# Optimization experiments

Measured on AMD Instinct MI355X. Metric: run time of the kernel, lower is better.

The kernel has to match this reference:

```python
import jax, jax.numpy as jnp
import numpy as np

H = 400          # hidden_layers
D_CUR = 3 + 2 + 50   # X_CUR + X_WIN + X_ET
D_AC = 3 + 49        # X_AC + X_T
D_AP = 6 + 49        # X_AP + X_T


def _cell(x, h1, c1, h2, c2, Wx, U, b):
    """2-child child-sum LSTM cell (inferred CustomLSTMCell).
    x: [T, in]; h*/c*: [T, H]; Wx: [in, 4H]; U: [H, 4H]; b: [4H].
    Gate order: i, f, o, u. f uses a per-child recurrent term.
    """
    g = x @ Wx + b                            # [T, 4H]
    gi, gf, go, gu = jnp.split(g, 4, axis=-1)
    Ui, Uf, Uo, Uu = jnp.split(U, 4, axis=-1)
    hs = h1 + h2
    i = jax.nn.sigmoid(gi + hs @ Ui)
    f1 = jax.nn.sigmoid(gf + h1 @ Uf)
    f2 = jax.nn.sigmoid(gf + h2 @ Uf)
    o = jax.nn.sigmoid(go + hs @ Uo)
    u = jnp.tanh(gu + hs @ Uu)
    c = i * u + f1 * c1 + f2 * c2
    return o * jnp.tanh(c), c


def setup_inputs() -> dict:
    key = jax.random.key(0)
    T, IN = 8192, 55
    ks = iter(jax.random.split(key, 40))

    def p(*shape):
        return jax.random.normal(next(ks), shape, dtype=jnp.float32) * 0.05

    inp = {
        "x_temp": jax.random.normal(next(ks), (T, IN), dtype=jnp.float32),
        "x_air": jax.random.normal(next(ks), (T, IN), dtype=jnp.float32),
    }
    for name, d_in in [("t1", IN), ("t2", H), ("t3", H), ("a1", IN), ("a2", H), ("a3", H)]:
        inp[f"Wx_{name}"] = p(d_in, 4 * H)
        inp[f"U_{name}"] = p(H, 4 * H)
        inp[f"b_{name}"] = p(4 * H)
    inp["W_cur"] = p(2 * H, D_CUR); inp["b_cur"] = p(D_CUR)
    inp["W_ac"] = p(H, D_AC);       inp["b_ac"] = p(D_AC)
    inp["W_ap"] = p(H, D_AP);       inp["b_ap"] = p(D_AP)
    return inp


def reference(x_temp, x_air,
              Wx_t1, U_t1, b_t1, Wx_t2, U_t2, b_t2, Wx_t3, U_t3, b_t3,
              Wx_a1, U_a1, b_a1, Wx_a2, U_a2, b_a2, Wx_a3, U_a3, b_a3,
              W_cur, b_cur, W_ac, b_ac, W_ap, b_ap):
    T = x_temp.shape[0]
    z = jnp.zeros((T, H), dtype=x_temp.dtype)
    # States are re-zeroed every timestep in the original loop, so all
    # timesteps are independent and we batch them along axis 0.
    ht, ct = _cell(x_temp, z, z, z, z, Wx_t1, U_t1, b_t1)
    ha, ca = _cell(x_air,  z, z, z, z, Wx_a1, U_a1, b_a1)
    ht2, ct2 = _cell(ht, ht, ct, ha, ca, Wx_t2, U_t2, b_t2)
    ha2, ca2 = _cell(ha, ht, ct, ha, ca, Wx_a2, U_a2, b_a2)
    ht3, _ = _cell(ht2, ht2, ct2, ha2, ca2, Wx_t3, U_t3, b_t3)
    ha3, _ = _cell(ha2, ht2, ct2, ha2, ca2, Wx_a3, U_a3, b_a3)
    out_cur_win_t = jnp.concatenate([ht3, ha3], axis=-1) @ W_cur + b_cur  # [T, 55]
    out_ac_tet = ht3 @ W_ac + b_ac                                        # [T, 52]
    out_ap_aet = ha3 @ W_ap + b_ap                                        # [T, 55]
    return out_cur_win_t, out_ac_tet, out_ap_aet
```

## Files before the change

### kernel.cpp

```cpp
#include <hip/hip_runtime.h>
#include <hip/hip_bf16.h>

typedef unsigned short u16;
typedef unsigned int u32;
typedef unsigned long long u64;
typedef __attribute__((ext_vector_type(4))) float f32x4;
typedef __attribute__((ext_vector_type(8))) short s16x8;

__device__ inline u16 f2bf(float f) {
  union { float f; u32 u; } v; v.f = f;
  u32 r = (v.u + 0x7FFFu + ((v.u >> 16) & 1u)) >> 16;
  return (u16)r;
}
__device__ inline float bf2f(u16 h) { return __uint_as_float((u32)h << 16); }
__device__ inline float sigf(float x) { return 1.0f / (1.0f + __expf(-x)); }
__device__ inline float tanhf_(float x) {
  float ax = fabsf(x);
  float e = __expf(-2.0f * ax);
  float r = (1.0f - e) / (1.0f + e);
  return copysignf(r, x);
}
__device__ inline f32x4 ld4bf(const u16* p) {
  u64 v = *(const u64*)p;
  f32x4 r;
  r.x = __uint_as_float((u32)(v & 0xFFFFu) << 16);
  r.y = __uint_as_float((u32)((v >> 16) & 0xFFFFu) << 16);
  r.z = __uint_as_float((u32)((v >> 32) & 0xFFFFu) << 16);
  r.w = __uint_as_float((u32)((v >> 48) & 0xFFFFu) << 16);
  return r;
}
__device__ inline void gload16(const u16* g, u16* l) {
  __builtin_amdgcn_global_load_lds(
      (const __attribute__((address_space(1))) void*)(g),
      (__attribute__((address_space(3))) void*)(l), 16, 0, 0);
}

#define GLD 4096

__global__ void zero_pads(u16* __restrict__ A1, u16* __restrict__ A2,
                          u16* __restrict__ A3) {
  int idx = blockIdx.x * 256 + threadIdx.x;
  if (idx >= 196608) return;
  int b = idx / 65536, r = idx % 65536;
  int t = r / 8, q = r % 8;
  u16* A = (b == 0) ? A1 : (b == 1) ? A2 : A3;
  *(u64*)(A + (size_t)t * 832 + 800 + q * 4) = 0ULL;
}

__global__ void pad_cast(const float* __restrict__ src, u16* __restrict__ dst,
                         int srcCols, int dstCols, int rows) {
  int idx = blockIdx.x * 256 + threadIdx.x;
  if (idx >= rows * dstCols) return;
  int r = idx / dstCols, c = idx % dstCols;
  float v = (c < srcCols) ? src[r * srcCols + c] : 0.f;
  dst[idx] = f2bf(v);
}

__global__ void transpose_cast(const float* __restrict__ src, u16* __restrict__ dst,
                               int srcK, int srcN) {
  int idx = blockIdx.x * 256 + threadIdx.x;
  if (idx >= 64 * 1664) return;
  int k = idx / 1664, n = idx % 1664;
  float v = (k < srcK && n < srcN) ? src[k * srcN + n] : 0.f;
  dst[n * 64 + k] = f2bf(v);
}

__global__ __launch_bounds__(256) void build_cell_B(
    const float* __restrict__ WxT, const float* __restrict__ UT,
    const float* __restrict__ WxA, const float* __restrict__ UA,
    u16* __restrict__ dst) {
  __shared__ float tile[64][65];
  const int np0 = blockIdx.x * 64;
  const int r0 = blockIdx.y * 64;
  const int tx = threadIdx.x & 63, ty = threadIdx.x >> 6;

  const int np = np0 + tx;
  const int cell = np >> 11;
  const int n = np & 2047;
  const float* Wx = cell ? WxA : WxT;
  const float* U  = cell ? UA  : UT;
  int g = 0, j = 0, gc = 0;
  if (n < 2000) {
    g = n / 400; j = n % 400;
    gc = (g == 0) ? j : (g <= 2) ? 400 + j : (g == 3) ? 800 + j : 1200 + j;
  }
#pragma unroll
  for (int it = 0; it < 16; ++it) {
    int r = r0 + it * 4 + ty;
    float v = 0.f;
    if (n < 2000 && r < 800) {
      bool htside = (r < 400);
      int rr = htside ? r : r - 400;
      float wx = Wx[rr * 1600 + gc];
      float uu = U [rr * 1600 + gc];
      if (cell == 0) {
        if (htside) v = (g == 2) ? wx : wx + uu;
        else        v = (g == 1) ? 0.f : uu;
      } else {
        if (htside) v = (g == 2) ? 0.f : uu;
        else        v = (g == 1) ? wx : wx + uu;
      }
    }
    tile[tx][it * 4 + ty] = v;
  }
  __syncthreads();
#pragma unroll
  for (int it = 0; it < 16; ++it) {
    int npw = np0 + it * 4 + ty;
    dst[(size_t)npw * 832 + r0 + tx] = f2bf(tile[it * 4 + ty][tx]);
  }
}

__global__ void build_proj_B(const float* __restrict__ Wcur, const float* __restrict__ Wac,
                             const float* __restrict__ Wap, u16* __restrict__ dst) {
  int idx = blockIdx.x * 256 + threadIdx.x;
  if (idx >= 256 * 832) return;
  int n = idx / 832, r = idx % 832;
  float v = 0.f;
  if (r < 800) {
    if (n < 55) v = Wcur[r * 55 + n];
    else if (n < 107) { if (r < 400) v = Wac[r * 52 + (n - 55)]; }
    else if (n < 162) { if (r >= 400) v = Wap[(r - 400) * 55 + (n - 107)]; }
  }
  dst[idx] = f2bf(v);
}

__global__ __launch_bounds__(256) void gemm_lds(
    const u16* __restrict__ A, const u16* __restrict__ Bt,
    u16* __restrict__ C, int K, int ldc) {
  __shared__ u16 As[128 * 64];
  __shared__ u16 Bs[128 * 64];
  const int tid = threadIdx.x;
  const int lane = tid & 63;
  const int wid = tid >> 6;

  const int nwg = gridDim.x * gridDim.y;
  const int bid = blockIdx.y * gridDim.x + blockIdx.x;
  const int swz = (bid & 7) * (nwg >> 3) + (bid >> 3);
  const int m0 = (swz / gridDim.x) * 128;
  const int n0 = (swz % gridDim.x) * 128;

  const int wm = (wid >> 1) << 6;
  const int wn = (wid & 1) << 6;

  f32x4 acc[4][4];
#pragma unroll
  for (int i = 0; i < 4; ++i)
#pragma unroll
    for (int j = 0; j < 4; ++j) acc[i][j] = (f32x4){0.f, 0.f, 0.f, 0.f};

  const int nkt = K >> 6;
  const int l8 = lane >> 3, lb = lane & 7;
  const int scol = (lb ^ l8) << 3;
  const u16* gA = A + (size_t)(m0 + wid * 8 + l8) * K + scol;
  const u16* gB = Bt + (size_t)(n0 + wid * 8 + l8) * K + scol;
  u16* lA = As + wid * 8 * 64;
  u16* lB = Bs + wid * 8 * 64;

  const int kq = (lane >> 4) << 3;
  const int rrow = lane & 15;

  for (int kt = 0; kt < nkt; ++kt) {
    __syncthreads();
    const u16* pa = gA + kt * 64;
    const u16* pb = gB + kt * 64;
#pragma unroll
    for (int c = 0; c < 4; ++c) {
      gload16(pa + (size_t)(c * 32) * K, lA + c * 2048);
      gload16(pb + (size_t)(c * 32) * K, lB + c * 2048);
    }
    __syncthreads();
#pragma unroll
    for (int half = 0; half < 2; ++half) {
      const int kk = half * 32 + kq;
      s16x8 af[4], bfr[4];
#pragma unroll
      for (int f = 0; f < 4; ++f) {
        int ar = wm + f * 16 + rrow;
        af[f] = *(const s16x8*)((const char*)As + ar * 128 + ((kk * 2) ^ ((ar & 7) << 4)));
        int br = wn + f * 16 + rrow;
        bfr[f] = *(const s16x8*)((const char*)Bs + br * 128 + ((kk * 2) ^ ((br & 7) << 4)));
      }
#pragma unroll
      for (int i = 0; i < 4; ++i)
#pragma unroll
        for (int j = 0; j < 4; ++j)
          acc[i][j] = __builtin_amdgcn_mfma_f32_16x16x32_bf16(af[i], bfr[j], acc[i][j], 0, 0, 0);
    }
  }

  const int crow0 = m0 + wm + ((lane >> 4) << 2);
  const int ccol0 = n0 + wn + rrow;
#pragma unroll
  for (int i = 0; i < 4; ++i)
#pragma unroll
    for (int j = 0; j < 4; ++j)
#pragma unroll
      for (int r = 0; r < 4; ++r)
        C[(size_t)(crow0 + i * 16 + r) * ldc + (ccol0 + j * 16)] = f2bf(acc[i][j][r]);
}

#define PK 832
#define PNKT 13
#define ABY 32768
#define BBY 16384
#define BUFB 49152

__global__ __launch_bounds__(512, 2) void gemm_pipe(
    const u16* __restrict__ A, const u16* __restrict__ Bt,
    u16* __restrict__ C, int ldc) {
  __shared__ char sm[3 * BUFB];
  const int tid = threadIdx.x;
  const int lane = tid & 63;
  const int wid = tid >> 6;

  const int nwg = gridDim.x * gridDim.y;
  const int bid = blockIdx.y * gridDim.x + blockIdx.x;
  const int swz = (bid & 7) * (nwg >> 3) + (bid >> 3);
  const int m0 = (swz / gridDim.x) * 256;
  const int n0 = (swz % gridDim.x) * 128;

  const int wr = wid >> 1;
  const int wc = wid & 1;

  f32x4 acc[4][4];
#pragma unroll
  for (int i = 0; i < 4; ++i)
#pragma unroll
    for (int j = 0; j < 4; ++j) acc[i][j] = (f32x4){0.f, 0.f, 0.f, 0.f};

  const int q = lane >> 3, lb = lane & 7;
  const int scol = (lb ^ q) << 3;
  const u16* gA = A + (size_t)(m0 + wid * 8 + q) * PK + scol;
  const u16* gB = Bt + (size_t)(n0 + wid * 8 + q) * PK + scol;
  const int wrow = wid * 8;

  const int kq = (lane >> 4) << 3;
  const int rrow = lane & 15;

#define STAGE(kt, buf)                                                        \
  {                                                                           \
    char* bb = sm + (buf) * BUFB;                                             \
    const u16* pa = gA + (kt) * 64;                                           \
    const u16* pb = gB + (kt) * 64;                                           \
    gload16(pa,                  (u16*)(bb + (0 * 64 + wrow) * 128));         \
    gload16(pa + 64 * PK,        (u16*)(bb + (1 * 64 + wrow) * 128));         \
    gload16(pa + 128 * PK,       (u16*)(bb + (2 * 64 + wrow) * 128));         \
    gload16(pa + 192 * PK,       (u16*)(bb + (3 * 64 + wrow) * 128));         \
    gload16(pb,                  (u16*)(bb + ABY + (0 * 64 + wrow) * 128));   \
    gload16(pb + 64 * PK,        (u16*)(bb + ABY + (1 * 64 + wrow) * 128));   \
  }

  STAGE(0, 0);
  STAGE(1, 1);

  int cbuf = 0;
  int sbuf = 2;
  for (int k = 0; k < PNKT; ++k) {
    __builtin_amdgcn_sched_barrier(0);
    __builtin_amdgcn_s_barrier();
    if (k < PNKT - 2) {
      STAGE(k + 2, sbuf);
      asm volatile("s_waitcnt vmcnt(12)" ::: "memory");
    } else if (k == PNKT - 2) {
      asm volatile("s_waitcnt vmcnt(6)" ::: "memory");
    } else {
      asm volatile("s_waitcnt vmcnt(0)" ::: "memory");
    }
    __builtin_amdgcn_s_barrier();
    __builtin_amdgcn_sched_barrier(0);

    const char* bb = sm + cbuf * BUFB;
    s16x8 af[4][2], bfr[4][2];
#pragma unroll
    for (int i = 0; i < 4; ++i) {
      int ar = wr * 64 + i * 16 + rrow;
      const char* base = bb + ar * 128;
#pragma unroll
      for (int h = 0; h < 2; ++h) {
        int kk2 = (h * 32 + kq) * 2;
        af[i][h] = *(const s16x8*)(base + (kk2 ^ ((ar & 7) << 4)));
      }
    }
#pragma unroll
    for (int jf = 0; jf < 4; ++jf) {
      int br = wc * 64 + jf * 16 + rrow;
      const char* base = bb + ABY + br * 128;
#pragma unroll
      for (int h = 0; h < 2; ++h) {
        int kk2 = (h * 32 + kq) * 2;
        bfr[jf][h] = *(const s16x8*)(base + (kk2 ^ ((br & 7) << 4)));
      }
    }
#pragma unroll
    for (int i = 0; i < 4; ++i)
#pragma unroll
      for (int jf = 0; jf < 4; ++jf)
#pragma unroll
        for (int h = 0; h < 2; ++h)
          acc[i][jf] = __builtin_amdgcn_mfma_f32_16x16x32_bf16(
              af[i][h], bfr[jf][h], acc[i][jf], 0, 0, 0);

    cbuf = (cbuf == 2) ? 0 : cbuf + 1;
    sbuf = (sbuf == 2) ? 0 : sbuf + 1;
  }
#undef STAGE

  const int crow0 = m0 + wr * 64 + ((lane >> 4) << 2);
  const int ccol0 = n0 + wc * 64 + rrow;
#pragma unroll
  for (int i = 0; i < 4; ++i)
#pragma unroll
    for (int jf = 0; jf < 4; ++jf)
#pragma unroll
      for (int r = 0; r < 4; ++r)
        C[(size_t)(crow0 + i * 16 + r) * ldc + (ccol0 + jf * 16)] = f2bf(acc[i][jf][r]);
}

__global__ void ep1(const u16* __restrict__ G,
                    const float* __restrict__ bT, const float* __restrict__ bA,
                    u16* __restrict__ Aout,
                    float* __restrict__ CT, float* __restrict__ CA) {
  int idx = blockIdx.x * 256 + threadIdx.x;
  if (idx >= 8192 * 200) return;
  int t = idx / 200, r = idx % 200;
  int cell = r / 100, j0 = (r % 100) * 4;
  const u16* g = G + (size_t)t * GLD + cell * 2048;
  const float* b = cell ? bA : bT;
  float* Cout = cell ? CA : CT;
  f32x4 ip = ld4bf(g + j0);
  f32x4 op = ld4bf(g + 800 + j0);
  f32x4 up = ld4bf(g + 1200 + j0);
  u64 hv = 0;
  f32x4 cv;
#pragma unroll
  for (int k = 0; k < 4; ++k) {
    int j = j0 + k;
    float c = sigf(ip[k] + b[j]) * tanhf_(up[k] + b[1200 + j]);
    float h = sigf(op[k] + b[800 + j]) * tanhf_(c);
    cv[k] = c;
    hv |= (u64)f2bf(h) << (16 * k);
  }
  *(u64*)(Aout + (size_t)t * 832 + cell * 400 + j0) = hv;
  *(f32x4*)(Cout + (size_t)t * 400 + j0) = cv;
}

__global__ void ep2(const u16* __restrict__ G,
                    const float* __restrict__ bT, const float* __restrict__ bA,
                    const float* __restrict__ C1, const float* __restrict__ C2,
                    u16* __restrict__ Aout,
                    float* __restrict__ CT, float* __restrict__ CA) {
  int idx = blockIdx.x * 256 + threadIdx.x;
  if (idx >= 8192 * 200) return;
  int t = idx / 200, r = idx % 200;
  int cell = r / 100, j0 = (r % 100) * 4;
  const u16* g = G + (size_t)t * GLD + cell * 2048;
  const float* b = cell ? bA : bT;
  float* Cout = cell ? CA : CT;
  f32x4 ip  = ld4bf(g + j0);
  f32x4 f1p = ld4bf(g + 400 + j0);
  f32x4 f2p = ld4bf(g + 800 + j0);
  f32x4 op  = ld4bf(g + 1200 + j0);
  f32x4 up  = ld4bf(g + 1600 + j0);
  f32x4 c1 = *(const f32x4*)(C1 + (size_t)t * 400 + j0);
  f32x4 c2 = *(const f32x4*)(C2 + (size_t)t * 400 + j0);
  u64 hv = 0;
  f32x4 cv;
#pragma unroll
  for (int k = 0; k < 4; ++k) {
    int j = j0 + k;
    float c = sigf(ip[k] + b[j]) * tanhf_(up[k] + b[1200 + j])
            + sigf(f1p[k] + b[400 + j]) * c1[k]
            + sigf(f2p[k] + b[400 + j]) * c2[k];
    float h = sigf(op[k] + b[800 + j]) * tanhf_(c);
    cv[k] = c;
    hv |= (u64)f2bf(h) << (16 * k);
  }
  *(u64*)(Aout + (size_t)t * 832 + cell * 400 + j0) = hv;
  if (Cout) *(f32x4*)(Cout + (size_t)t * 400 + j0) = cv;
}

__global__ void ep_out(const u16* __restrict__ G,
                       const float* __restrict__ bcur, const float* __restrict__ bac,
                       const float* __restrict__ bap, float* __restrict__ out) {
  int idx = blockIdx.x * 256 + threadIdx.x;
  if (idx >= 8192 * 162) return;
  int t = idx / 162, j = idx % 162;
  float v = bf2f(G[(size_t)t * GLD + j]);
  if (j < 55)       out[t * 55 + j] = v + bcur[j];
  else if (j < 107) out[450560 + t * 52 + (j - 55)] = v + bac[j - 55];
  else              out[876544 + t * 55 + (j - 107)] = v + bap[j - 107];
}

extern "C" void kernel_launch(void* const* d_in, const int* in_sizes, int n_in,
                              void* d_out, int out_size, void* d_ws, size_t ws_size,
                              hipStream_t stream) {
  const float* x_temp = (const float*)d_in[0];
  const float* x_air  = (const float*)d_in[1];
  const float* Wx_t1  = (const float*)d_in[2];
  const float* b_t1   = (const float*)d_in[4];
  const float* Wx_t2  = (const float*)d_in[5];
  const float* U_t2   = (const float*)d_in[6];
  const float* b_t2   = (const float*)d_in[7];
  const float* Wx_t3  = (const float*)d_in[8];
  const float* U_t3   = (const float*)d_in[9];
  const float* b_t3   = (const float*)d_in[10];
  const float* Wx_a1  = (const float*)d_in[11];
  const float* b_a1   = (const float*)d_in[13];
  const float* Wx_a2  = (const float*)d_in[14];
  const float* U_a2   = (const float*)d_in[15];
  const float* b_a2   = (const float*)d_in[16];
  const float* Wx_a3  = (const float*)d_in[17];
  const float* U_a3   = (const float*)d_in[18];
  const float* b_a3   = (const float*)d_in[19];
  const float* W_cur  = (const float*)d_in[20];
  const float* b_cur  = (const float*)d_in[21];
  const float* W_ac   = (const float*)d_in[22];
  const float* b_ac   = (const float*)d_in[23];
  const float* W_ap   = (const float*)d_in[24];
  const float* b_ap   = (const float*)d_in[25];

  char* ws = (char*)d_ws;
  u16*   A0t = (u16*)(ws + 0);
  u16*   A0a = (u16*)(ws + 1048576);
  u16*   B1t = (u16*)(ws + 2097152);
  u16*   B1a = (u16*)(ws + 2310144);
  u16*   Bp  = (u16*)(ws + 2523136);
  u16*   A1  = (u16*)(ws + 2949120);
  u16*   A2  = (u16*)(ws + 16580608);
  u16*   A3  = (u16*)(ws + 30212096);
  float* Ct  = (float*)(ws + 43843584);
  float* Ca  = (float*)(ws + 56950784);
  float* C2t = (float*)(ws + 70057984);
  float* C2a = (float*)(ws + 83165184);
  u16*   B2  = (u16*)(ws + 96272384);
  u16*   B3  = (u16*)(ws + 103088128);
  u16*   G   = (u16*)(ws + 109903872);
  float* out = (float*)d_out;

  dim3 blk(256);
  zero_pads<<<768, blk, 0, stream>>>(A1, A2, A3);
  pad_cast<<<2048, blk, 0, stream>>>(x_temp, A0t, 55, 64, 8192);
  pad_cast<<<2048, blk, 0, stream>>>(x_air,  A0a, 55, 64, 8192);
  transpose_cast<<<416, blk, 0, stream>>>(Wx_t1, B1t, 55, 1600);
  transpose_cast<<<416, blk, 0, stream>>>(Wx_a1, B1a, 55, 1600);
  build_cell_B<<<dim3(64, 13), blk, 0, stream>>>(Wx_t2, U_t2, Wx_a2, U_a2, B2);
  build_cell_B<<<dim3(64, 13), blk, 0, stream>>>(Wx_t3, U_t3, Wx_a3, U_a3, B3);
  build_proj_B<<<832, blk, 0, stream>>>(W_cur, W_ac, W_ap, Bp);

  gemm_lds<<<dim3(13, 64), blk, 0, stream>>>(A0t, B1t, G, 64, GLD);
  gemm_lds<<<dim3(13, 64), blk, 0, stream>>>(A0a, B1a, G + 2048, 64, GLD);
  ep1<<<6400, blk, 0, stream>>>(G, b_t1, b_a1, A1, Ct, Ca);
  gemm_pipe<<<dim3(32, 32), dim3(512), 0, stream>>>(A1, B2, G, GLD);
  ep2<<<6400, blk, 0, stream>>>(G, b_t2, b_a2, Ct, Ca, A2, C2t, C2a);
  gemm_pipe<<<dim3(32, 32), dim3(512), 0, stream>>>(A2, B3, G, GLD);
  ep2<<<6400, blk, 0, stream>>>(G, b_t3, b_a3, C2t, C2a, A3, nullptr, nullptr);
  gemm_lds<<<dim3(2, 64), blk, 0, stream>>>(A3, Bp, G, 832, GLD);
  ep_out<<<5184, blk, 0, stream>>>(G, b_cur, b_ac, b_ap, out);
}
```

Measured before the change: 407.2 us.

## Interleave global prefetch with MFMA sub-phases and stage GEMM epilogue through LDS

```diff
diff --git a/kernel.cpp b/kernel.cpp
--- a/kernel.cpp
+++ b/kernel.cpp
@@ -6,6 +6,7 @@
 typedef unsigned long long u64;
 typedef __attribute__((ext_vector_type(4))) float f32x4;
 typedef __attribute__((ext_vector_type(8))) short s16x8;
+typedef __attribute__((ext_vector_type(4))) int i32x4;
 
 __device__ inline u16 f2bf(float f) {
   union { float f; u32 u; } v; v.f = f;
@@ -201,12 +202,11 @@
 }
 
 #define PK 832
-#define PNKT 13
+#define NKT 13
 #define ABY 32768
-#define BBY 16384
 #define BUFB 49152
 
-__global__ __launch_bounds__(512, 2) void gemm_pipe(
+__global__ __launch_bounds__(512, 2) void gemm_256(
     const u16* __restrict__ A, const u16* __restrict__ Bt,
     u16* __restrict__ C, int ldc) {
   __shared__ char sm[3 * BUFB];
@@ -235,86 +235,132 @@
   const u16* gB = Bt + (size_t)(n0 + wid * 8 + q) * PK + scol;
   const int wrow = wid * 8;
 
+#define CHA(kt, buf, c) gload16(gA + (kt) * 64 + (size_t)((c) * 64) * PK,      \
+                                (u16*)(sm + (buf) * BUFB + ((c) * 64 + wrow) * 128))
+#define CHB(kt, buf, c) gload16(gB + (kt) * 64 + (size_t)((c) * 64) * PK,      \
+                                (u16*)(sm + (buf) * BUFB + ABY + ((c) * 64 + wrow) * 128))
+
   const int kq = (lane >> 4) << 3;
   const int rrow = lane & 15;
 
-#define STAGE(kt, buf)                                                        \
-  {                                                                           \
-    char* bb = sm + (buf) * BUFB;                                             \
-    const u16* pa = gA + (kt) * 64;                                           \
-    const u16* pb = gB + (kt) * 64;                                           \
-    gload16(pa,                  (u16*)(bb + (0 * 64 + wrow) * 128));         \
-    gload16(pa + 64 * PK,        (u16*)(bb + (1 * 64 + wrow) * 128));         \
-    gload16(pa + 128 * PK,       (u16*)(bb + (2 * 64 + wrow) * 128));         \
-    gload16(pa + 192 * PK,       (u16*)(bb + (3 * 64 + wrow) * 128));         \
-    gload16(pb,                  (u16*)(bb + ABY + (0 * 64 + wrow) * 128));   \
-    gload16(pb + 64 * PK,        (u16*)(bb + ABY + (1 * 64 + wrow) * 128));   \
-  }
-
-  STAGE(0, 0);
-  STAGE(1, 1);
-
-  int cbuf = 0;
-  int sbuf = 2;
-  for (int k = 0; k < PNKT; ++k) {
-    __builtin_amdgcn_sched_barrier(0);
-    __builtin_amdgcn_s_barrier();
-    if (k < PNKT - 2) {
-      STAGE(k + 2, sbuf);
-      asm volatile("s_waitcnt vmcnt(12)" ::: "memory");
-    } else if (k == PNKT - 2) {
-      asm volatile("s_waitcnt vmcnt(6)" ::: "memory");
-    } else {
-      asm volatile("s_waitcnt vmcnt(0)" ::: "memory");
-    }
-    __builtin_amdgcn_s_barrier();
-    __builtin_amdgcn_sched_barrier(0);
-
-    const char* bb = sm + cbuf * BUFB;
-    s16x8 af[4][2], bfr[4][2];
-#pragma unroll
-    for (int i = 0; i < 4; ++i) {
+  CHA(0, 0, 0); CHA(0, 0, 1); CHA(0, 0, 2); CHA(0, 0, 3);
+  CHB(0, 0, 0); CHB(0, 0, 1);
+  CHA(1, 1, 0); CHA(1, 1, 1); CHA(1, 1, 2); CHA(1, 1, 3);
+  CHB(1, 1, 0); CHB(1, 1, 1);
+  asm volatile("s_waitcnt vmcnt(6)" ::: "memory");
+  __builtin_amdgcn_sched_barrier(0);
+  __builtin_amdgcn_s_barrier();
+  __builtin_amdgcn_sched_barrier(0);
+
+  int cur = 0;
+  for (int t = 0; t < NKT; ++t) {
+    const char* bb = sm + cur * BUFB;
+    const int sb = (cur == 0) ? 2 : cur - 1;
+    const bool st = (t + 2) < NKT;
+    s16x8 bfr[4][2];
+
+    {
+#pragma unroll
+      for (int jf = 0; jf < 4; ++jf) {
+        int br = wc * 64 + jf * 16 + rrow;
+        const char* base = bb + ABY + br * 128;
+#pragma unroll
+        for (int h = 0; h < 2; ++h)
+          bfr[jf][h] = *(const s16x8*)(base + (((h * 32 + kq) * 2) ^ ((br & 7) << 4)));
+      }
+      int ar = wr * 64 + rrow;
+      const char* abase = bb + ar * 128;
+      s16x8 af0 = *(const s16x8*)(abase + ((kq * 2) ^ ((ar & 7) << 4)));
+      s16x8 af1 = *(const s16x8*)(abase + (((32 + kq) * 2) ^ ((ar & 7) << 4)));
+      if (st) { CHA(t + 2, sb, 0); CHA(t + 2, sb, 1); }
+      __builtin_amdgcn_sched_barrier(0);
+      __builtin_amdgcn_s_barrier();
+      __builtin_amdgcn_sched_barrier(0);
+      __builtin_amdgcn_s_setprio(1);
+#pragma unroll
+      for (int jf = 0; jf < 4; ++jf) {
+        acc[0][jf] = __builtin_amdgcn_mfma_f32_16x16x32_bf16(af0, bfr[jf][0], acc[0][jf], 0, 0, 0);
+        acc[0][jf] = __builtin_amdgcn_mfma_f32_16x16x32_bf16(af1, bfr[jf][1], acc[0][jf], 0, 0, 0);
+      }
+      __builtin_amdgcn_s_setprio(0);
+      __builtin_amdgcn_sched_barrier(0);
+      __builtin_amdgcn_s_barrier();
+      __builtin_amdgcn_sched_barrier(0);
+    }
+#pragma unroll
+    for (int i = 1; i < 3; ++i) {
       int ar = wr * 64 + i * 16 + rrow;
-      const char* base = bb + ar * 128;
-#pragma unroll
-      for (int h = 0; h < 2; ++h) {
-        int kk2 = (h * 32 + kq) * 2;
-        af[i][h] = *(const s16x8*)(base + (kk2 ^ ((ar & 7) << 4)));
-      }
-    }
-#pragma unroll
-    for (int jf = 0; jf < 4; ++jf) {
-      int br = wc * 64 + jf * 16 + rrow;
-      const char* base = bb + ABY + br * 128;
-#pragma unroll
-      for (int h = 0; h < 2; ++h) {
-        int kk2 = (h * 32 + kq) * 2;
-        bfr[jf][h] = *(const s16x8*)(base + (kk2 ^ ((br & 7) << 4)));
-      }
-    }
-#pragma unroll
-    for (int i = 0; i < 4; ++i)
-#pragma unroll
-      for (int jf = 0; jf < 4; ++jf)
-#pragma unroll
-        for (int h = 0; h < 2; ++h)
-          acc[i][jf] = __builtin_amdgcn_mfma_f32_16x16x32_bf16(
-              af[i][h], bfr[jf][h], acc[i][jf], 0, 0, 0);
-
-    cbuf = (cbuf == 2) ? 0 : cbuf + 1;
-    sbuf = (sbuf == 2) ? 0 : sbuf + 1;
-  }
-#undef STAGE
-
-  const int crow0 = m0 + wr * 64 + ((lane >> 4) << 2);
-  const int ccol0 = n0 + wc * 64 + rrow;
+      const char* abase = bb + ar * 128;
+      s16x8 af0 = *(const s16x8*)(abase + ((kq * 2) ^ ((ar & 7) << 4)));
+      s16x8 af1 = *(const s16x8*)(abase + (((32 + kq) * 2) ^ ((ar & 7) << 4)));
+      if (st) {
+        if (i == 1) { CHA(t + 2, sb, 2); CHA(t + 2, sb, 3); }
+        else        { CHB(t + 2, sb, 0); }
+      }
+      __builtin_amdgcn_sched_barrier(0);
+      __builtin_amdgcn_s_barrier();
+      __builtin_amdgcn_sched_barrier(0);
+      __builtin_amdgcn_s_setprio(1);
+#pragma unroll
+      for (int jf = 0; jf < 4; ++jf) {
+        acc[i][jf] = __builtin_amdgcn_mfma_f32_16x16x32_bf16(af0, bfr[jf][0], acc[i][jf], 0, 0, 0);
+        acc[i][jf] = __builtin_amdgcn_mfma_f32_16x16x32_bf16(af1, bfr[jf][1], acc[i][jf], 0, 0, 0);
+      }
+      __builtin_amdgcn_s_setprio(0);
+      __builtin_amdgcn_sched_barrier(0);
+      __builtin_amdgcn_s_barrier();
+      __builtin_amdgcn_sched_barrier(0);
+    }
+    {
+      int ar = wr * 64 + 48 + rrow;
+      const char* abase = bb + ar * 128;
+      s16x8 af0 = *(const s16x8*)(abase + ((kq * 2) ^ ((ar & 7) << 4)));
+      s16x8 af1 = *(const s16x8*)(abase + (((32 + kq) * 2) ^ ((ar & 7) << 4)));
+      if (st) {
+        CHB(t + 2, sb, 1);
+        asm volatile("s_waitcnt vmcnt(6)" ::: "memory");
+      } else {
+        asm volatile("s_waitcnt vmcnt(0)" ::: "memory");
+      }
+      __builtin_amdgcn_sched_barrier(0);
+      __builtin_amdgcn_s_barrier();
+      __builtin_amdgcn_sched_barrier(0);
+      __builtin_amdgcn_s_setprio(1);
+#pragma unroll
+      for (int jf = 0; jf < 4; ++jf) {
+        acc[3][jf] = __builtin_amdgcn_mfma_f32_16x16x32_bf16(af0, bfr[jf][0], acc[3][jf], 0, 0, 0);
+        acc[3][jf] = __builtin_amdgcn_mfma_f32_16x16x32_bf16(af1, bfr[jf][1], acc[3][jf], 0, 0, 0);
+      }
+      __builtin_amdgcn_s_setprio(0);
+      __builtin_amdgcn_sched_barrier(0);
+      __builtin_amdgcn_s_barrier();
+      __builtin_amdgcn_sched_barrier(0);
+    }
+    cur = (cur == 2) ? 0 : cur + 1;
+  }
+#undef CHA
+#undef CHB
+
+  u16* eps = (u16*)(sm + wid * 8192);
 #pragma unroll
   for (int i = 0; i < 4; ++i)
 #pragma unroll
     for (int jf = 0; jf < 4; ++jf)
 #pragma unroll
-      for (int r = 0; r < 4; ++r)
-        C[(size_t)(crow0 + i * 16 + r) * ldc + (ccol0 + jf * 16)] = f2bf(acc[i][jf][r]);
+      for (int r = 0; r < 4; ++r) {
+        int row = i * 16 + ((lane >> 4) << 2) + r;
+        int colb = (jf * 16 + rrow) * 2;
+        *(u16*)((char*)eps + row * 128 + (colb ^ ((row & 7) << 4))) = f2bf(acc[i][jf][r]);
+      }
+  const size_t crowW = m0 + wr * 64;
+  const int ccolW = n0 + wc * 64;
+#pragma unroll
+  for (int p = 0; p < 8; ++p) {
+    int row = p * 8 + (lane >> 3);
+    int segb = (lane & 7) * 16;
+    i32x4 v = *(const i32x4*)((char*)eps + row * 128 + (segb ^ ((row & 7) << 4)));
+    *(i32x4*)(C + (crowW + row) * (size_t)ldc + ccolW + (lane & 7) * 8) = v;
+  }
 }
 
 __global__ void ep1(const u16* __restrict__ G,
@@ -351,33 +397,37 @@
                     u16* __restrict__ Aout,
                     float* __restrict__ CT, float* __restrict__ CA) {
   int idx = blockIdx.x * 256 + threadIdx.x;
-  if (idx >= 8192 * 200) return;
-  int t = idx / 200, r = idx % 200;
-  int cell = r / 100, j0 = (r % 100) * 4;
-  const u16* g = G + (size_t)t * GLD + cell * 2048;
-  const float* b = cell ? bA : bT;
-  float* Cout = cell ? CA : CT;
-  f32x4 ip  = ld4bf(g + j0);
-  f32x4 f1p = ld4bf(g + 400 + j0);
-  f32x4 f2p = ld4bf(g + 800 + j0);
-  f32x4 op  = ld4bf(g + 1200 + j0);
-  f32x4 up  = ld4bf(g + 1600 + j0);
+  if (idx >= 8192 * 100) return;
+  int t = idx / 100, j0 = (idx % 100) * 4;
   f32x4 c1 = *(const f32x4*)(C1 + (size_t)t * 400 + j0);
   f32x4 c2 = *(const f32x4*)(C2 + (size_t)t * 400 + j0);
-  u64 hv = 0;
-  f32x4 cv;
-#pragma unroll
-  for (int k = 0; k < 4; ++k) {
-    int j = j0 + k;
-    float c = sigf(ip[k] + b[j]) * tanhf_(up[k] + b[1200 + j])
-            + sigf(f1p[k] + b[400 + j]) * c1[k]
-            + sigf(f2p[k] + b[400 + j]) * c2[k];
-    float h = sigf(op[k] + b[800 + j]) * tanhf_(c);
-    cv[k] = c;
-    hv |= (u64)f2bf(h) << (16 * k);
-  }
-  *(u64*)(Aout + (size_t)t * 832 + cell * 400 + j0) = hv;
-  if (Cout) *(f32x4*)(Cout + (size_t)t * 400 + j0) = cv;
+#pragma unroll
+  for (int cell = 0; cell < 2; ++cell) {
+    const u16* g = G + (size_t)t * GLD + cell * 2048;
+    const float* b = cell ? bA : bT;
+    f32x4 ip  = ld4bf(g + j0);
+    f32x4 f1p = ld4bf(g + 400 + j0);
+    f32x4 f2p = ld4bf(g + 800 + j0);
+    f32x4 op  = ld4bf(g + 1200 + j0);
+    f32x4 up  = ld4bf(g + 1600 + j0);
+    u64 hv = 0;
+    f32x4 cv;
+#pragma unroll
+    for (int k = 0; k < 4; ++k) {
+      int j = j0 + k;
+      float c = sigf(ip[k] + b[j]) * tanhf_(up[k] + b[1200 + j])
+              + sigf(f1p[k] + b[400 + j]) * c1[k]
+              + sigf(f2p[k] + b[400 + j]) * c2[k];
+      float h = sigf(op[k] + b[800 + j]) * tanhf_(c);
+      cv[k] = c;
+      hv |= (u64)f2bf(h) << (16 * k);
+    }
+    *(u64*)(Aout + (size_t)t * 832 + cell * 400 + j0) = hv;
+    if (CT) {
+      float* Cout = cell ? CA : CT;
+      *(f32x4*)(Cout + (size_t)t * 400 + j0) = cv;
+    }
+  }
 }
 
 __global__ void ep_out(const u16* __restrict__ G,
@@ -451,10 +501,10 @@
   gemm_lds<<<dim3(13, 64), blk, 0, stream>>>(A0t, B1t, G, 64, GLD);
   gemm_lds<<<dim3(13, 64), blk, 0, stream>>>(A0a, B1a, G + 2048, 64, GLD);
   ep1<<<6400, blk, 0, stream>>>(G, b_t1, b_a1, A1, Ct, Ca);
-  gemm_pipe<<<dim3(32, 32), dim3(512), 0, stream>>>(A1, B2, G, GLD);
-  ep2<<<6400, blk, 0, stream>>>(G, b_t2, b_a2, Ct, Ca, A2, C2t, C2a);
-  gemm_pipe<<<dim3(32, 32), dim3(512), 0, stream>>>(A2, B3, G, GLD);
-  ep2<<<6400, blk, 0, stream>>>(G, b_t3, b_a3, C2t, C2a, A3, nullptr, nullptr);
+  gemm_256<<<dim3(32, 32), dim3(512), 0, stream>>>(A1, B2, G, GLD);
+  ep2<<<3200, blk, 0, stream>>>(G, b_t2, b_a2, Ct, Ca, A2, C2t, C2a);
+  gemm_256<<<dim3(32, 32), dim3(512), 0, stream>>>(A2, B3, G, GLD);
+  ep2<<<3200, blk, 0, stream>>>(G, b_t3, b_a3, C2t, C2a, A3, nullptr, nullptr);
   gemm_lds<<<dim3(2, 64), blk, 0, stream>>>(A3, Bp, G, 832, GLD);
   ep_out<<<5184, blk, 0, stream>>>(G, b_cur, b_ac, b_ap, out);
 }
```

After: 383.5 us. 5.8% less time.
